# Optimization experiments

Measured on AMD Instinct MI355X. Metric: run time of the kernel, lower is better.

Reference implementation:

```python
import jax, jax.numpy as jnp
import numpy as np

N_HEAD = 16
ROPE_THETA = 10000.0


def setup_inputs() -> dict:
    key = jax.random.key(0)
    k0, k1, k2 = jax.random.split(key, 3)
    B, T, C = 2, 2048, 1024
    s = 0.02  # GPT-2 style init scale
    return {
        "x": jax.random.normal(k0, (B, T, C), jnp.float32),
        "w_attn": jax.random.normal(k1, (C, 3 * C), jnp.float32) * s,
        "b_attn": jnp.zeros((3 * C,), jnp.float32),
        "w_proj": jax.random.normal(k2, (C, C), jnp.float32) * s,
        "b_proj": jnp.zeros((C,), jnp.float32),
    }


def _rope(x):
    # x: [B, H, T, D]; interleaved-pair rotary (lucidrains rotate_queries_or_keys)
    T, D = x.shape[-2], x.shape[-1]
    inv_freq = 1.0 / (ROPE_THETA ** (jnp.arange(0, D, 2, dtype=jnp.float32) / D))
    freqs = jnp.arange(T, dtype=jnp.float32)[:, None] * inv_freq[None, :]  # [T, D/2]
    emb = jnp.repeat(freqs, 2, axis=-1)  # [T, D], each freq duplicated per pair
    cos, sin = jnp.cos(emb), jnp.sin(emb)
    xr = x.reshape(*x.shape[:-1], D // 2, 2)
    x1, x2 = xr[..., 0], xr[..., 1]
    rot = jnp.stack((-x2, x1), axis=-1).reshape(x.shape)  # rotate_half
    return x * cos + rot * sin


def reference(x, w_attn, b_attn, w_proj, b_proj):
    B, T, C = x.shape
    H = N_HEAD
    D = C // H
    qkv = x @ w_attn + b_attn                      # [B, T, 3C]
    q, k, v = jnp.split(qkv, 3, axis=-1)

    def heads(t):
        return t.reshape(B, T, H, D).transpose(0, 2, 1, 3)  # [B, H, T, D]

    q, k, v = heads(q), heads(k), heads(v)
    q = _rope(q)
    k = _rope(k)

    att = jnp.einsum("bhqd,bhkd->bhqk", q, k) * (1.0 / np.sqrt(D))
    causal = jnp.tril(jnp.ones((T, T), dtype=bool))
    att = jnp.where(causal, att, -jnp.inf)
    att = jax.nn.softmax(att, axis=-1)
    y = jnp.einsum("bhqk,bhkd->bhqd", att, v)
    y = y.transpose(0, 2, 1, 3).reshape(B, T, C)
    return y @ w_proj + b_proj
```

## Files before the change

kernel.cpp:

```cpp
#include <hip/hip_runtime.h>
#include <hip/hip_bf16.h>
#include <stdint.h>

typedef __hip_bfloat16 bf16;
typedef __attribute__((ext_vector_type(8))) short bf16x8;
typedef __attribute__((ext_vector_type(4))) float f32x4;

__device__ inline float bf2f(bf16 v) { return __bfloat162float(v); }
__device__ inline bf16 f2bf(float f) { return __float2bfloat16(f); }

__device__ inline void glds16(const void* g, void* l) {
    __builtin_amdgcn_global_load_lds(
        (const __attribute__((address_space(1))) uint32_t*)g,
        (__attribute__((address_space(3))) uint32_t*)l, 16, 0, 0);
}

__device__ inline void conv_wt_tile(const float* __restrict__ W,
                                    bf16* __restrict__ Wt, int N, int K,
                                    int bx, int by, int tid, bf16 (*t)[72])
{
    const int n0 = bx * 64, k0 = by * 64;
#pragma unroll
    for (int p = 0; p < 4; ++p) {
        int idx = p * 256 + tid;
        int kr = idx >> 4, c4 = idx & 15;
        float4 f = *(const float4*)(W + (size_t)(k0 + kr) * N + n0 + c4 * 4);
        t[kr][c4 * 4 + 0] = f2bf(f.x); t[kr][c4 * 4 + 1] = f2bf(f.y);
        t[kr][c4 * 4 + 2] = f2bf(f.z); t[kr][c4 * 4 + 3] = f2bf(f.w);
    }
    __syncthreads();
#pragma unroll
    for (int p = 0; p < 2; ++p) {
        int idx = p * 256 + tid;
        int nr = idx >> 3, ch = idx & 7;
        union { bf16x8 v; bf16 e[8]; } u;
#pragma unroll
        for (int j = 0; j < 8; ++j) u.e[j] = t[ch * 8 + j][nr];
        *(bf16x8*)(Wt + (size_t)(n0 + nr) * K + k0 + ch * 8) = u.v;
    }
}

__global__ __launch_bounds__(256) void prep(
    const float* __restrict__ x, bf16* __restrict__ xbf,
    const float* __restrict__ w_attn, bf16* __restrict__ wat,
    const float* __restrict__ w_proj, bf16* __restrict__ wpt,
    float2* __restrict__ tab)
{
    __shared__ bf16 t[64][72];
    const int bid = blockIdx.x;
    const int tid = threadIdx.x;
    if (bid < 2048) {
        size_t i = ((size_t)bid * 256 + tid) * 8;
        float4 f0 = *(const float4*)(x + i);
        float4 f1 = *(const float4*)(x + i + 4);
        union { bf16x8 v; bf16 e[8]; } u;
        u.e[0] = f2bf(f0.x); u.e[1] = f2bf(f0.y); u.e[2] = f2bf(f0.z); u.e[3] = f2bf(f0.w);
        u.e[4] = f2bf(f1.x); u.e[5] = f2bf(f1.y); u.e[6] = f2bf(f1.z); u.e[7] = f2bf(f1.w);
        *(bf16x8*)(xbf + i) = u.v;
    } else if (bid < 2816) {
        int idx = bid - 2048;
        conv_wt_tile(w_attn, wat, 3072, 1024, idx % 48, idx / 48, tid, t);
    } else if (bid < 3072) {
        int idx = bid - 2816;
        conv_wt_tile(w_proj, wpt, 1024, 1024, idx % 16, idx / 16, tid, t);
    } else {
        int gid = (bid - 3072) * 256 + tid;
        int p = gid & 31, tt = gid >> 5;
        float invf = expf(-(float)(2 * p) * (9.210340371976184f / 64.0f));
        float sn, cs;
        sincosf((float)tt * invf, &sn, &cs);
        tab[gid] = make_float2(cs, sn);
    }
}

template <bool OUTF32>
__global__ __launch_bounds__(256) void gemm_bt(
    const bf16* __restrict__ A, const bf16* __restrict__ Bt,
    const float* __restrict__ bias, int M, int N, int K, void* __restrict__ outv)
{
    __shared__ __align__(16) bf16 sa[128 * 64];
    __shared__ __align__(16) bf16 sb[128 * 64];

    const int tid  = threadIdx.x;
    const int wave = tid >> 6, lane = tid & 63;
    const int quad = lane >> 4, l16 = lane & 15;
    const int wm = wave >> 1, wn = wave & 1;
    const int row0 = blockIdx.x * 128, n0 = blockIdx.y * 128;

    f32x4 acc[4][4] = {};

    const int srow = lane >> 3;
    const int schk = lane & 7;

    for (int k0 = 0; k0 < K; k0 += 64) {
        __syncthreads();
#pragma unroll
        for (int half = 0; half < 2; ++half) {
#pragma unroll
            for (int g = 0; g < 2; ++g) {
                int rowb = half * 64 + wave * 16 + g * 8;
                int row  = rowb + srow;
                glds16(A + (size_t)(row0 + row) * K + k0 + ((schk ^ row) & 7) * 8,
                       &sa[rowb * 64]);
                glds16(Bt + (size_t)(n0 + row) * K + k0 + ((schk ^ row) & 7) * 8,
                       &sb[rowb * 64]);
            }
        }
        __syncthreads();

#pragma unroll
        for (int kk = 0; kk < 2; ++kk) {
            bf16x8 af[4], bfr[4];
#pragma unroll
            for (int mi = 0; mi < 4; ++mi) {
                int row = wm * 64 + mi * 16 + l16;
                af[mi] = *(const bf16x8*)&sa[row * 64 + (((kk * 4 + quad) ^ row) & 7) * 8];
            }
#pragma unroll
            for (int ni = 0; ni < 4; ++ni) {
                int row = wn * 64 + ni * 16 + l16;
                bfr[ni] = *(const bf16x8*)&sb[row * 64 + (((kk * 4 + quad) ^ row) & 7) * 8];
            }
#pragma unroll
            for (int mi = 0; mi < 4; ++mi)
#pragma unroll
                for (int ni = 0; ni < 4; ++ni)
                    acc[mi][ni] = __builtin_amdgcn_mfma_f32_16x16x32_bf16(
                        af[mi], bfr[ni], acc[mi][ni], 0, 0, 0);
        }
    }

#pragma unroll
    for (int ni = 0; ni < 4; ++ni) {
        int col = n0 + wn * 64 + ni * 16 + l16;
        float bvv = bias[col];
#pragma unroll
        for (int mi = 0; mi < 4; ++mi) {
#pragma unroll
            for (int r = 0; r < 4; ++r) {
                int row = row0 + wm * 64 + mi * 16 + quad * 4 + r;
                float v = acc[mi][ni][r] + bvv;
                if (OUTF32) ((float*)outv)[(size_t)row * N + col] = v;
                else        ((bf16*)outv)[(size_t)row * N + col] = f2bf(v);
            }
        }
    }
}

__global__ __launch_bounds__(256) void gemm_qkv(
    const bf16* __restrict__ A, const bf16* __restrict__ Bt,
    const float* __restrict__ bias, const float2* __restrict__ tab,
    bf16* __restrict__ qh, bf16* __restrict__ kh, bf16* __restrict__ vc)
{
    const int K = 1024;
    __shared__ __align__(16) bf16 sa[128 * 64];
    __shared__ __align__(16) bf16 sb[128 * 64];

    const int tid  = threadIdx.x;
    const int wave = tid >> 6, lane = tid & 63;
    const int quad = lane >> 4, l16 = lane & 15;
    const int wm = wave >> 1, wn = wave & 1;
    const int row0 = blockIdx.x * 128, n0 = blockIdx.y * 128;

    f32x4 acc[4][4] = {};

    const int srow = lane >> 3;
    const int schk = lane & 7;

    for (int k0 = 0; k0 < K; k0 += 64) {
        __syncthreads();
#pragma unroll
        for (int half = 0; half < 2; ++half) {
#pragma unroll
            for (int g = 0; g < 2; ++g) {
                int rowb = half * 64 + wave * 16 + g * 8;
                int row  = rowb + srow;
                glds16(A + (size_t)(row0 + row) * K + k0 + ((schk ^ row) & 7) * 8,
                       &sa[rowb * 64]);
                glds16(Bt + (size_t)(n0 + row) * K + k0 + ((schk ^ row) & 7) * 8,
                       &sb[rowb * 64]);
            }
        }
        __syncthreads();

#pragma unroll
        for (int kk = 0; kk < 2; ++kk) {
            bf16x8 af[4], bfr[4];
#pragma unroll
            for (int mi = 0; mi < 4; ++mi) {
                int row = wm * 64 + mi * 16 + l16;
                af[mi] = *(const bf16x8*)&sa[row * 64 + (((kk * 4 + quad) ^ row) & 7) * 8];
            }
#pragma unroll
            for (int ni = 0; ni < 4; ++ni) {
                int row = wn * 64 + ni * 16 + l16;
                bfr[ni] = *(const bf16x8*)&sb[row * 64 + (((kk * 4 + quad) ^ row) & 7) * 8];
            }
#pragma unroll
            for (int mi = 0; mi < 4; ++mi)
#pragma unroll
                for (int ni = 0; ni < 4; ++ni)
                    acc[mi][ni] = __builtin_amdgcn_mfma_f32_16x16x32_bf16(
                        af[mi], bfr[ni], acc[mi][ni], 0, 0, 0);
        }
    }

    const float QS = 0.125f * 1.44269504088896f;
#pragma unroll
    for (int ni = 0; ni < 4; ++ni) {
        int col = n0 + wn * 64 + ni * 16 + l16;
        float bvv = bias[col];
        int sec = col >> 10;
        int cd  = col & 1023;
        int h   = cd >> 6, d = cd & 63;
        int p   = d >> 1;
        bool odd = (d & 1) != 0;
#pragma unroll
        for (int mi = 0; mi < 4; ++mi) {
#pragma unroll
            for (int r = 0; r < 4; ++r) {
                int row = row0 + wm * 64 + mi * 16 + quad * 4 + r;
                float v = acc[mi][ni][r] + bvv;
                float vp = __shfl_xor(v, 1);
                if (sec == 2) {
                    vc[(size_t)row * 1024 + cd] = f2bf(v);
                } else {
                    int tt = row & 2047, b = row >> 11;
                    float2 cssn = tab[tt * 32 + p];
                    float ro = odd ? (v * cssn.x + vp * cssn.y)
                                   : (v * cssn.x - vp * cssn.y);
                    size_t dst = (((size_t)(b * 16 + h)) * 2048 + tt) * 64 + d;
                    if (sec == 0) qh[dst] = f2bf(ro * QS);
                    else          kh[dst] = f2bf(ro);
                }
            }
        }
    }
}

__global__ __launch_bounds__(256) void transpose_v(
    const bf16* __restrict__ vc, bf16* __restrict__ vt)
{
    __shared__ bf16 t[64][72];
    const int t0 = blockIdx.x * 64;
    const int bh = blockIdx.y, b = bh >> 4, h = bh & 15;
    const int tid = threadIdx.x;
#pragma unroll
    for (int p = 0; p < 2; ++p) {
        int idx = p * 256 + tid;
        int tr = idx >> 3, ch = idx & 7;
        bf16x8 v = *(const bf16x8*)(vc + ((size_t)(b * 2048 + t0 + tr)) * 1024
                                    + h * 64 + ch * 8);
#pragma unroll
        for (int j = 0; j < 8; ++j) t[tr][ch * 8 + j] = ((const bf16*)&v)[j];
    }
    __syncthreads();
#pragma unroll
    for (int p = 0; p < 2; ++p) {
        int idx = p * 256 + tid;
        int dr = idx >> 3, ch = idx & 7;
        union { bf16x8 v; bf16 e[8]; } u;
#pragma unroll
        for (int j = 0; j < 8; ++j) u.e[j] = t[ch * 8 + j][dr];
        *(bf16x8*)(vt + ((size_t)bh * 64 + dr) * 2048 + t0 + ch * 8) = u.v;
    }
}

__global__ __launch_bounds__(256) void attn_k(
    const bf16* __restrict__ qg, const bf16* __restrict__ kg,
    const bf16* __restrict__ vtg, bf16* __restrict__ y)
{
    __shared__ __align__(16) bf16 sK[128 * 64];
    __shared__ __align__(16) bf16 sV[64 * 128];
    __shared__ __align__(16) bf16 pL[4][16][136];

    const int tid  = threadIdx.x;
    const int wave = tid >> 6, lane = tid & 63;
    const int quad = lane >> 4, l16 = lane & 15;
    const int bh   = blockIdx.x;
    const int qt   = 31 - (int)blockIdx.y;
    const bf16* Q  = qg  + (size_t)bh * 2048 * 64;
    const bf16* K  = kg  + (size_t)bh * 2048 * 64;
    const bf16* Vt = vtg + (size_t)bh * 64 * 2048;
    const int b = bh >> 4, h = bh & 15;

    const int q0 = qt * 64 + wave * 16;

    bf16x8 aq[2];
    aq[0] = *(const bf16x8*)(Q + (size_t)(q0 + l16) * 64 + quad * 8);
    aq[1] = *(const bf16x8*)(Q + (size_t)(q0 + l16) * 64 + 32 + quad * 8);

    union { bf16x8 v; short e[8]; } uo;
#pragma unroll
    for (int j = 0; j < 8; ++j) uo.e[j] = (short)0x3F80;
    const bf16x8 vones = uo.v;

    f32x4 o[4] = {};
    f32x4 ls   = {};
    float m_r[4] = {-1e30f, -1e30f, -1e30f, -1e30f};
    const float THR = 8.0f;

    for (int kt = 0; kt <= q0 + 15; kt += 128) {
        __syncthreads();
#pragma unroll
        for (int c = 0; c < 4; ++c) {
            int key = wave * 32 + c * 8 + (lane >> 3);
            int p = lane & 7;
            glds16(K + (size_t)(kt + key) * 64 + ((p ^ key) & 7) * 8,
                   &sK[(wave * 32 + c * 8) * 64]);
        }
#pragma unroll
        for (int c = 0; c < 4; ++c) {
            int d = wave * 16 + c * 4 + (lane >> 4);
            int p = lane & 15;
            glds16(Vt + (size_t)d * 2048 + kt + ((p ^ d) & 15) * 8,
                   &sV[(wave * 16 + c * 4) * 128]);
        }
        __syncthreads();

        const int nlast = min(7, (q0 - kt) >> 4);
        f32x4 sc[8];
        __builtin_amdgcn_s_setprio(1);
#pragma unroll
        for (int nt = 0; nt < 8; ++nt) {
            if (nt > nlast) continue;
            int key = nt * 16 + l16;
            f32x4 s0 = {};
            bf16x8 bk0 = *(const bf16x8*)&sK[key * 64 + ((quad ^ key) & 7) * 8];
            s0 = __builtin_amdgcn_mfma_f32_16x16x32_bf16(aq[0], bk0, s0, 0, 0, 0);
            bf16x8 bk1 = *(const bf16x8*)&sK[key * 64 + (((4 + quad) ^ key) & 7) * 8];
            sc[nt] = __builtin_amdgcn_mfma_f32_16x16x32_bf16(aq[1], bk1, s0, 0, 0, 0);
        }
        __builtin_amdgcn_s_setprio(0);
        {
            const int diag = (q0 - kt) >> 4;
            if (diag <= 7) {
                int key = kt + diag * 16 + l16;
#pragma unroll
                for (int r = 0; r < 4; ++r) {
                    int row = q0 + quad * 4 + r;
                    if (key > row) sc[diag][r] = -1e30f;
                }
            }
        }
        float rowmax[4] = {-1e30f, -1e30f, -1e30f, -1e30f};
#pragma unroll
        for (int nt = 0; nt < 8; ++nt) {
            if (nt > nlast) continue;
#pragma unroll
            for (int r = 0; r < 4; ++r) rowmax[r] = fmaxf(rowmax[r], sc[nt][r]);
        }
        bool okl = (rowmax[0] <= m_r[0] + THR) && (rowmax[1] <= m_r[1] + THR) &&
                   (rowmax[2] <= m_r[2] + THR) && (rowmax[3] <= m_r[3] + THR);
        if (!__all((int)okl)) {
#pragma unroll
            for (int off = 1; off < 16; off <<= 1)
#pragma unroll
                for (int r = 0; r < 4; ++r)
                    rowmax[r] = fmaxf(rowmax[r], __shfl_xor(rowmax[r], off));
            float alpha[4];
#pragma unroll
            for (int r = 0; r < 4; ++r) {
                float mn = fmaxf(m_r[r], rowmax[r]);
                alpha[r] = exp2f(m_r[r] - mn);
                m_r[r] = mn;
            }
#pragma unroll
            for (int nt = 0; nt < 4; ++nt)
#pragma unroll
                for (int r = 0; r < 4; ++r) o[nt][r] *= alpha[r];
#pragma unroll
            for (int r = 0; r < 4; ++r) ls[r] *= alpha[r];
        }
#pragma unroll
        for (int nt = 0; nt < 8; ++nt) {
            if (nt > nlast) continue;
#pragma unroll
            for (int r = 0; r < 4; ++r) sc[nt][r] = exp2f(sc[nt][r] - m_r[r]);
        }

#pragma unroll
        for (int nt = 0; nt < 8; ++nt) {
            if (nt > nlast) continue;
            int blk = (2 * nt + (l16 >> 3)) ^ quad;
#pragma unroll
            for (int r = 0; r < 4; ++r)
                pL[wave][quad * 4 + r][blk * 8 + (l16 & 7)] = f2bf(sc[nt][r]);
        }
        if (nlast < 7 && !(nlast & 1)) {
            int blk = (2 * (nlast + 1) + (l16 >> 3)) ^ quad;
#pragma unroll
            for (int r = 0; r < 4; ++r)
                pL[wave][quad * 4 + r][blk * 8 + (l16 & 7)] = f2bf(0.f);
        }
        __builtin_amdgcn_s_setprio(1);
#pragma unroll
        for (int c = 0; c < 4; ++c) {
            if (c > (nlast >> 1)) continue;
            bf16x8 pa = *(const bf16x8*)&pL[wave][l16][(((4 * c + quad) ^ (l16 >> 2)) * 8)];
            ls = __builtin_amdgcn_mfma_f32_16x16x32_bf16(pa, vones, ls, 0, 0, 0);
#pragma unroll
            for (int dnt = 0; dnt < 4; ++dnt) {
                int d = dnt * 16 + l16;
                int cc = c * 4 + quad;
                bf16x8 vb = *(const bf16x8*)&sV[d * 128 + ((cc ^ d) & 15) * 8];
                o[dnt] = __builtin_amdgcn_mfma_f32_16x16x32_bf16(pa, vb, o[dnt], 0, 0, 0);
            }
        }
        __builtin_amdgcn_s_setprio(0);
    }

#pragma unroll
    for (int r = 0; r < 4; ++r) {
        float inv = 1.0f / ls[r];
        int qq = q0 + quad * 4 + r;
#pragma unroll
        for (int nt = 0; nt < 4; ++nt) {
            int d = nt * 16 + l16;
            y[((size_t)(b * 2048 + qq)) * 1024 + h * 64 + d] = f2bf(o[nt][r] * inv);
        }
    }
}

extern "C" void kernel_launch(void* const* d_in, const int* in_sizes, int n_in,
                              void* d_out, int out_size, void* d_ws, size_t ws_size,
                              hipStream_t stream) {
    const float* x      = (const float*)d_in[0];
    const float* w_attn = (const float*)d_in[1];
    const float* b_attn = (const float*)d_in[2];
    const float* w_proj = (const float*)d_in[3];
    const float* b_proj = (const float*)d_in[4];
    float* out = (float*)d_out;

    bf16* xbf = (bf16*)d_ws;
    bf16* wat = xbf + (size_t)4194304;
    bf16* wpt = wat + (size_t)3145728;
    float2* tab = (float2*)(wpt + (size_t)1048576);
    bf16* qh  = wpt + (size_t)1048576 + 262144;
    bf16* kh  = qh  + (size_t)4194304;
    bf16* vc  = kh  + (size_t)4194304;
    bf16* vt  = vc  + (size_t)4194304;
    bf16* yws = vt  + (size_t)4194304;

    dim3 blk(256);
    prep<<<dim3(3328), blk, 0, stream>>>(x, xbf, w_attn, wat, w_proj, wpt, tab);
    gemm_qkv<<<dim3(32, 24), blk, 0, stream>>>(xbf, wat, b_attn, tab, qh, kh, vc);
    transpose_v<<<dim3(32, 32), blk, 0, stream>>>(vc, vt);
    attn_k<<<dim3(32, 32), blk, 0, stream>>>(qh, kh, vt, yws);
    gemm_bt<true><<<dim3(32, 8), blk, 0, stream>>>(yws, wpt, b_proj,
                                                   4096, 1024, 1024, out);
    (void)in_sizes; (void)n_in; (void)ws_size; (void)out_size;
}
```

Baseline: 232.6 us.

## Fuse V transpose into QKV GEMM epilogue and retile output projection GEMM

The QKV GEMM epilogue now writes V straight into the head-major transposed layout as 4-element bf16 vectors. This removes the separate transpose_v kernel and its round trip of V through global memory. The output projection moves to a dedicated kernel with 64x128 tiles, so it launches 512 blocks instead of 256 and fills more CUs. The transposed V stores are strided 8-byte writes, which could coalesce worse, and the smaller projection tiles reuse each loaded tile less.

```diff
diff --git a/kernel.cpp b/kernel.cpp
--- a/kernel.cpp
+++ b/kernel.cpp
@@ -4,6 +4,7 @@
 
 typedef __hip_bfloat16 bf16;
 typedef __attribute__((ext_vector_type(8))) short bf16x8;
+typedef __attribute__((ext_vector_type(4))) short bf16x4;
 typedef __attribute__((ext_vector_type(4))) float f32x4;
 
 __device__ inline float bf2f(bf16 v) { return __bfloat162float(v); }
@@ -73,11 +74,12 @@
     }
 }
 
-template <bool OUTF32>
-__global__ __launch_bounds__(256) void gemm_bt(
+__global__ __launch_bounds__(256) void gemm_qkv(
     const bf16* __restrict__ A, const bf16* __restrict__ Bt,
-    const float* __restrict__ bias, int M, int N, int K, void* __restrict__ outv)
+    const float* __restrict__ bias, const float2* __restrict__ tab,
+    bf16* __restrict__ qh, bf16* __restrict__ kh, bf16* __restrict__ vt)
 {
+    const int K = 1024;
     __shared__ __align__(16) bf16 sa[128 * 64];
     __shared__ __align__(16) bf16 sb[128 * 64];
 
@@ -130,81 +132,6 @@
         }
     }
 
-#pragma unroll
-    for (int ni = 0; ni < 4; ++ni) {
-        int col = n0 + wn * 64 + ni * 16 + l16;
-        float bvv = bias[col];
-#pragma unroll
-        for (int mi = 0; mi < 4; ++mi) {
-#pragma unroll
-            for (int r = 0; r < 4; ++r) {
-                int row = row0 + wm * 64 + mi * 16 + quad * 4 + r;
-                float v = acc[mi][ni][r] + bvv;
-                if (OUTF32) ((float*)outv)[(size_t)row * N + col] = v;
-                else        ((bf16*)outv)[(size_t)row * N + col] = f2bf(v);
-            }
-        }
-    }
-}
-
-__global__ __launch_bounds__(256) void gemm_qkv(
-    const bf16* __restrict__ A, const bf16* __restrict__ Bt,
-    const float* __restrict__ bias, const float2* __restrict__ tab,
-    bf16* __restrict__ qh, bf16* __restrict__ kh, bf16* __restrict__ vc)
-{
-    const int K = 1024;
-    __shared__ __align__(16) bf16 sa[128 * 64];
-    __shared__ __align__(16) bf16 sb[128 * 64];
-
-    const int tid  = threadIdx.x;
-    const int wave = tid >> 6, lane = tid & 63;
-    const int quad = lane >> 4, l16 = lane & 15;
-    const int wm = wave >> 1, wn = wave & 1;
-    const int row0 = blockIdx.x * 128, n0 = blockIdx.y * 128;
-
-    f32x4 acc[4][4] = {};
-
-    const int srow = lane >> 3;
-    const int schk = lane & 7;
-
-    for (int k0 = 0; k0 < K; k0 += 64) {
-        __syncthreads();
-#pragma unroll
-        for (int half = 0; half < 2; ++half) {
-#pragma unroll
-            for (int g = 0; g < 2; ++g) {
-                int rowb = half * 64 + wave * 16 + g * 8;
-                int row  = rowb + srow;
-                glds16(A + (size_t)(row0 + row) * K + k0 + ((schk ^ row) & 7) * 8,
-                       &sa[rowb * 64]);
-                glds16(Bt + (size_t)(n0 + row) * K + k0 + ((schk ^ row) & 7) * 8,
-                       &sb[rowb * 64]);
-            }
-        }
-        __syncthreads();
-
-#pragma unroll
-        for (int kk = 0; kk < 2; ++kk) {
-            bf16x8 af[4], bfr[4];
-#pragma unroll
-            for (int mi = 0; mi < 4; ++mi) {
-                int row = wm * 64 + mi * 16 + l16;
-                af[mi] = *(const bf16x8*)&sa[row * 64 + (((kk * 4 + quad) ^ row) & 7) * 8];
-            }
-#pragma unroll
-            for (int ni = 0; ni < 4; ++ni) {
-                int row = wn * 64 + ni * 16 + l16;
-                bfr[ni] = *(const bf16x8*)&sb[row * 64 + (((kk * 4 + quad) ^ row) & 7) * 8];
-            }
-#pragma unroll
-            for (int mi = 0; mi < 4; ++mi)
-#pragma unroll
-                for (int ni = 0; ni < 4; ++ni)
-                    acc[mi][ni] = __builtin_amdgcn_mfma_f32_16x16x32_bf16(
-                        af[mi], bfr[ni], acc[mi][ni], 0, 0, 0);
-        }
-    }
-
     const float QS = 0.125f * 1.44269504088896f;
 #pragma unroll
     for (int ni = 0; ni < 4; ++ni) {
@@ -213,18 +140,26 @@
         int sec = col >> 10;
         int cd  = col & 1023;
         int h   = cd >> 6, d = cd & 63;
-        int p   = d >> 1;
-        bool odd = (d & 1) != 0;
-#pragma unroll
-        for (int mi = 0; mi < 4; ++mi) {
-#pragma unroll
-            for (int r = 0; r < 4; ++r) {
-                int row = row0 + wm * 64 + mi * 16 + quad * 4 + r;
-                float v = acc[mi][ni][r] + bvv;
-                float vp = __shfl_xor(v, 1);
-                if (sec == 2) {
-                    vc[(size_t)row * 1024 + cd] = f2bf(v);
-                } else {
+        if (sec == 2) {
+#pragma unroll
+            for (int mi = 0; mi < 4; ++mi) {
+                int trow = row0 + wm * 64 + mi * 16 + quad * 4;
+                int tt0 = trow & 2047, bb = trow >> 11;
+                union { bf16x4 v; bf16 e[4]; } pv;
+#pragma unroll
+                for (int r = 0; r < 4; ++r) pv.e[r] = f2bf(acc[mi][ni][r] + bvv);
+                *(bf16x4*)(vt + ((size_t)((bb * 16 + h) * 64 + d)) * 2048 + tt0) = pv.v;
+            }
+        } else {
+            int p   = d >> 1;
+            bool odd = (d & 1) != 0;
+#pragma unroll
+            for (int mi = 0; mi < 4; ++mi) {
+#pragma unroll
+                for (int r = 0; r < 4; ++r) {
+                    int row = row0 + wm * 64 + mi * 16 + quad * 4 + r;
+                    float v = acc[mi][ni][r] + bvv;
+                    float vp = __shfl_xor(v, 1);
                     int tt = row & 2047, b = row >> 11;
                     float2 cssn = tab[tt * 32 + p];
                     float ro = odd ? (v * cssn.x + vp * cssn.y)
@@ -238,31 +173,76 @@
     }
 }
 
-__global__ __launch_bounds__(256) void transpose_v(
-    const bf16* __restrict__ vc, bf16* __restrict__ vt)
+__global__ __launch_bounds__(256) void gemm_proj(
+    const bf16* __restrict__ A, const bf16* __restrict__ Bt,
+    const float* __restrict__ bias, float* __restrict__ out)
 {
-    __shared__ bf16 t[64][72];
-    const int t0 = blockIdx.x * 64;
-    const int bh = blockIdx.y, b = bh >> 4, h = bh & 15;
-    const int tid = threadIdx.x;
-#pragma unroll
-    for (int p = 0; p < 2; ++p) {
-        int idx = p * 256 + tid;
-        int tr = idx >> 3, ch = idx & 7;
-        bf16x8 v = *(const bf16x8*)(vc + ((size_t)(b * 2048 + t0 + tr)) * 1024
-                                    + h * 64 + ch * 8);
-#pragma unroll
-        for (int j = 0; j < 8; ++j) t[tr][ch * 8 + j] = ((const bf16*)&v)[j];
-    }
-    __syncthreads();
-#pragma unroll
-    for (int p = 0; p < 2; ++p) {
-        int idx = p * 256 + tid;
-        int dr = idx >> 3, ch = idx & 7;
-        union { bf16x8 v; bf16 e[8]; } u;
-#pragma unroll
-        for (int j = 0; j < 8; ++j) u.e[j] = t[ch * 8 + j][dr];
-        *(bf16x8*)(vt + ((size_t)bh * 64 + dr) * 2048 + t0 + ch * 8) = u.v;
+    const int N = 1024, K = 1024;
+    __shared__ __align__(16) bf16 sa[64 * 64];
+    __shared__ __align__(16) bf16 sb[128 * 64];
+
+    const int tid  = threadIdx.x;
+    const int wave = tid >> 6, lane = tid & 63;
+    const int quad = lane >> 4, l16 = lane & 15;
+    const int row0 = blockIdx.x * 64, n0 = blockIdx.y * 128;
+
+    f32x4 acc[4][2] = {};
+
+    const int srow = lane >> 3;
+    const int schk = lane & 7;
+
+    for (int k0 = 0; k0 < K; k0 += 64) {
+        __syncthreads();
+#pragma unroll
+        for (int g = 0; g < 2; ++g) {
+            int rowb = wave * 16 + g * 8;
+            int row  = rowb + srow;
+            glds16(A + (size_t)(row0 + row) * K + k0 + ((schk ^ row) & 7) * 8,
+                   &sa[rowb * 64]);
+        }
+#pragma unroll
+        for (int g = 0; g < 4; ++g) {
+            int rowb = wave * 32 + g * 8;
+            int row  = rowb + srow;
+            glds16(Bt + (size_t)(n0 + row) * K + k0 + ((schk ^ row) & 7) * 8,
+                   &sb[rowb * 64]);
+        }
+        __syncthreads();
+
+#pragma unroll
+        for (int kk = 0; kk < 2; ++kk) {
+            bf16x8 af[4], bfr[2];
+#pragma unroll
+            for (int mi = 0; mi < 4; ++mi) {
+                int row = mi * 16 + l16;
+                af[mi] = *(const bf16x8*)&sa[row * 64 + (((kk * 4 + quad) ^ row) & 7) * 8];
+            }
+#pragma unroll
+            for (int ni = 0; ni < 2; ++ni) {
+                int row = wave * 32 + ni * 16 + l16;
+                bfr[ni] = *(const bf16x8*)&sb[row * 64 + (((kk * 4 + quad) ^ row) & 7) * 8];
+            }
+#pragma unroll
+            for (int mi = 0; mi < 4; ++mi)
+#pragma unroll
+                for (int ni = 0; ni < 2; ++ni)
+                    acc[mi][ni] = __builtin_amdgcn_mfma_f32_16x16x32_bf16(
+                        af[mi], bfr[ni], acc[mi][ni], 0, 0, 0);
+        }
+    }
+
+#pragma unroll
+    for (int ni = 0; ni < 2; ++ni) {
+        int col = n0 + wave * 32 + ni * 16 + l16;
+        float bvv = bias[col];
+#pragma unroll
+        for (int mi = 0; mi < 4; ++mi) {
+#pragma unroll
+            for (int r = 0; r < 4; ++r) {
+                int row = row0 + mi * 16 + quad * 4 + r;
+                out[(size_t)row * N + col] = acc[mi][ni][r] + bvv;
+            }
+        }
     }
 }
 
@@ -438,16 +418,13 @@
     float2* tab = (float2*)(wpt + (size_t)1048576);
     bf16* qh  = wpt + (size_t)1048576 + 262144;
     bf16* kh  = qh  + (size_t)4194304;
-    bf16* vc  = kh  + (size_t)4194304;
-    bf16* vt  = vc  + (size_t)4194304;
+    bf16* vt  = kh  + (size_t)4194304;
     bf16* yws = vt  + (size_t)4194304;
 
     dim3 blk(256);
     prep<<<dim3(3328), blk, 0, stream>>>(x, xbf, w_attn, wat, w_proj, wpt, tab);
-    gemm_qkv<<<dim3(32, 24), blk, 0, stream>>>(xbf, wat, b_attn, tab, qh, kh, vc);
-    transpose_v<<<dim3(32, 32), blk, 0, stream>>>(vc, vt);
+    gemm_qkv<<<dim3(32, 24), blk, 0, stream>>>(xbf, wat, b_attn, tab, qh, kh, vt);
     attn_k<<<dim3(32, 32), blk, 0, stream>>>(qh, kh, vt, yws);
-    gemm_bt<true><<<dim3(32, 8), blk, 0, stream>>>(yws, wpt, b_proj,
-                                                   4096, 1024, 1024, out);
+    gemm_proj<<<dim3(64, 8), blk, 0, stream>>>(yws, wpt, b_proj, out);
     (void)in_sizes; (void)n_in; (void)ws_size; (void)out_size;
 }
```

Result: faster. 210.4 us (-9.5%).
